# Optimization experiments

Measured on AMD Instinct MI355X. Metric: run time of the kernel, lower is better.

## Reference

```python
import jax, jax.numpy as jnp
import numpy as np

N, E, D_IN, D_OUT, K = 50000, 800000, 128, 128, 3

def setup_inputs() -> dict:
    key = jax.random.key(0)
    k1, k2, k3, k4, k5 = jax.random.split(key, 5)
    feat = jax.random.normal(k1, (N, D_IN), dtype=jnp.float32)
    src = jax.random.randint(k2, (E,), 0, N)
    dst = jax.random.randint(k3, (E,), 0, N)
    theta = 0.1 * jax.random.normal(k4, (K + 1,), dtype=jnp.float32)
    # xavier-uniform-like linear weight [out, in]
    lim = float(np.sqrt(6.0 / (D_IN + D_OUT)))
    W = jax.random.uniform(k5, (D_OUT, D_IN), minval=-lim, maxval=lim, dtype=jnp.float32)
    return {"feat": feat, "src": src, "dst": dst, "theta": theta, "W": W}

def reference(feat, src, dst, theta, W):
    n = feat.shape[0]
    # in-degree per destination node, clamped to >= 1
    deg = jax.ops.segment_sum(jnp.ones_like(dst, dtype=feat.dtype), dst, num_segments=n)
    d_invsqrt = jnp.maximum(deg, 1.0) ** -0.5  # [N]
    d_invsqrt = d_invsqrt[:, None]

    def L_prime(x):
        # -D^{-1/2} A D^{-1/2} x  (A aggregates src -> dst)
        msg = (x * d_invsqrt)[src]                      # [E, D]
        agg = jax.ops.segment_sum(msg, dst, num_segments=n)
        return -agg * d_invsqrt

    k = theta.shape[0] - 1
    h = theta[0] * feat
    T_km2 = feat
    T_km1 = L_prime(feat)
    if k >= 1:
        h = h + theta[1] * (T_km1 + 1.0) * 0.5
    for order in range(2, k + 1):
        T_k = 2.0 * L_prime(T_km1) - T_km2
        h = h + theta[order] * (T_k + 1.0) * 0.5
        T_km2, T_km1 = T_km1, T_k

    out = h @ W.T  # linear, no bias
    return jax.nn.leaky_relu(out, negative_slope=0.01)
```

## Files before the change

### kernel.cpp

```cpp
#include <hip/hip_runtime.h>

#define NN 50000
#define EE 800000
#define D 128

static inline size_t align_up(size_t x, size_t a) { return (x + a - 1) & ~(a - 1); }

__device__ __forceinline__ unsigned pack_bf16(float a, float b) {
    unsigned ua = __float_as_uint(a), ub = __float_as_uint(b);
    unsigned ra = (ua + 0x7fffu + ((ua >> 16) & 1u)) >> 16;
    unsigned rb = (ub + 0x7fffu + ((ub >> 16) & 1u)) & 0xffff0000u;
    return ra | rb;
}
__device__ __forceinline__ float bf_lo(unsigned u) { return __uint_as_float(u << 16); }
__device__ __forceinline__ float bf_hi(unsigned u) { return __uint_as_float(u & 0xffff0000u); }

__global__ void deg_kernel(const int* __restrict__ dst, int* __restrict__ deg, int E) {
    int e = blockIdx.x * blockDim.x + threadIdx.x;
    if (e < E) atomicAdd(&deg[dst[e]], 1);
}

__global__ void dinv_kernel(const int* __restrict__ deg, float* __restrict__ dinv, int n) {
    int i = blockIdx.x * blockDim.x + threadIdx.x;
    if (i < n) {
        float d = (float)deg[i];
        dinv[i] = rsqrtf(d > 1.0f ? d : 1.0f);
    }
}

__global__ void scale_kernel(const float* __restrict__ feat, const float* __restrict__ dinv,
                             unsigned* __restrict__ featb, int n) {
    int idx = blockIdx.x * blockDim.x + threadIdx.x;
    if (idx >= n * 64) return;
    int i = idx >> 6;
    float di = dinv[i];
    float2 f = ((const float2*)feat)[idx];
    featb[idx] = pack_bf16(f.x * di, f.y * di);
}

__global__ void scan_blk_kernel(const int* __restrict__ deg, int* __restrict__ bscan,
                                int* __restrict__ btot, int n) {
    __shared__ int ws4[4];
    int tid = threadIdx.x, b = blockIdx.x;
    int i = b * 256 + tid;
    int v = (i < n) ? deg[i] : 0;
    int lane = tid & 63, w = tid >> 6;
    int sc = v;
    #pragma unroll
    for (int off = 1; off < 64; off <<= 1) {
        int t = __shfl_up(sc, off);
        if (lane >= off) sc += t;
    }
    if (lane == 63) ws4[w] = sc;
    __syncthreads();
    int woff = 0;
    #pragma unroll
    for (int k = 0; k < 4; ++k)
        if (k < w) woff += ws4[k];
    int inc = sc + woff;
    bscan[b * 256 + tid] = inc;
    if (tid == 255) btot[b] = inc;
}

__global__ void scan_top_kernel(int* __restrict__ btot, int nb) {
    __shared__ int ws4[4];
    int tid = threadIdx.x;
    int v = (tid < nb) ? btot[tid] : 0;
    int lane = tid & 63, w = tid >> 6;
    int sc = v;
    #pragma unroll
    for (int off = 1; off < 64; off <<= 1) {
        int t = __shfl_up(sc, off);
        if (lane >= off) sc += t;
    }
    if (lane == 63) ws4[w] = sc;
    __syncthreads();
    int woff = 0;
    #pragma unroll
    for (int k = 0; k < 4; ++k)
        if (k < w) woff += ws4[k];
    if (tid < nb) btot[tid] = sc + woff - v;
}

__global__ void scan_fix_kernel(const int* __restrict__ bscan, const int* __restrict__ btot,
                                const int* __restrict__ deg, int* __restrict__ rowptr,
                                int* __restrict__ cursor, int n) {
    int i = blockIdx.x * blockDim.x + threadIdx.x;
    if (i >= n) return;
    int inc = bscan[i] + btot[i >> 8];
    rowptr[i + 1] = inc;
    cursor[i] = inc - deg[i];
    if (i == 0) rowptr[0] = 0;
}

__global__ void scatter_kernel(const int* __restrict__ src, const int* __restrict__ dst,
                               int* __restrict__ cursor, int* __restrict__ csr_src, int E) {
    int e = blockIdx.x * blockDim.x + threadIdx.x;
    if (e < E) {
        int p = atomicAdd(&cursor[dst[e]], 1);
        csr_src[p] = src[e];
    }
}

template <int MODE>
__global__ __launch_bounds__(256) void agg_kernel(
    const int* __restrict__ rowptr, const int* __restrict__ csr_src,
    const float* __restrict__ dinv, const unsigned* __restrict__ Xb,
    const float* __restrict__ feat, const float* __restrict__ T1f,
    const float* __restrict__ T2f, const float* __restrict__ theta,
    float* __restrict__ outf, unsigned* __restrict__ outb, int n) {
    int wid = (blockIdx.x * blockDim.x + threadIdx.x) >> 6;
    int lane = threadIdx.x & 63;
    if (wid >= n) return;
    int half = lane >> 5;
    int hl = lane & 31;
    int beg = rowptr[wid];
    int end = rowptr[wid + 1];
    const uint2* X2 = (const uint2*)Xb;
    float a0 = 0.f, a1 = 0.f, a2 = 0.f, a3 = 0.f;
    for (int e0 = beg; e0 < end; e0 += 64) {
        int s = (e0 + lane < end) ? csr_src[e0 + lane] : 0;
        int cnt = min(64, end - e0);
        int j = 0;
        for (; j + 8 <= cnt; j += 8) {
            int s0 = __shfl(s, j + 0 + half);
            int s1 = __shfl(s, j + 2 + half);
            int s2 = __shfl(s, j + 4 + half);
            int s3 = __shfl(s, j + 6 + half);
            uint2 u0 = X2[(size_t)s0 * 32 + hl];
            uint2 u1 = X2[(size_t)s1 * 32 + hl];
            uint2 u2 = X2[(size_t)s2 * 32 + hl];
            uint2 u3 = X2[(size_t)s3 * 32 + hl];
            a0 += bf_lo(u0.x); a1 += bf_hi(u0.x); a2 += bf_lo(u0.y); a3 += bf_hi(u0.y);
            a0 += bf_lo(u1.x); a1 += bf_hi(u1.x); a2 += bf_lo(u1.y); a3 += bf_hi(u1.y);
            a0 += bf_lo(u2.x); a1 += bf_hi(u2.x); a2 += bf_lo(u2.y); a3 += bf_hi(u2.y);
            a0 += bf_lo(u3.x); a1 += bf_hi(u3.x); a2 += bf_lo(u3.y); a3 += bf_hi(u3.y);
        }
        for (; j + 2 <= cnt; j += 2) {
            int sj = __shfl(s, j + half);
            uint2 u = X2[(size_t)sj * 32 + hl];
            a0 += bf_lo(u.x); a1 += bf_hi(u.x); a2 += bf_lo(u.y); a3 += bf_hi(u.y);
        }
        if (j < cnt) {
            int sj = __shfl(s, j);
            if (half == 0) {
                uint2 u = X2[(size_t)sj * 32 + hl];
                a0 += bf_lo(u.x); a1 += bf_hi(u.x); a2 += bf_lo(u.y); a3 += bf_hi(u.y);
            }
        }
    }
    a0 += __shfl_xor(a0, 32);
    a1 += __shfl_xor(a1, 32);
    a2 += __shfl_xor(a2, 32);
    a3 += __shfl_xor(a3, 32);

    float di = dinv[wid];
    size_t row4 = (size_t)wid * 32 + hl;
    float r0, r1, r2, r3;
    if (MODE == 1) {
        r0 = -di * a0; r1 = -di * a1; r2 = -di * a2; r3 = -di * a3;
    } else if (MODE == 2) {
        float4 f = ((const float4*)feat)[row4];
        r0 = -2.f * di * a0 - f.x;
        r1 = -2.f * di * a1 - f.y;
        r2 = -2.f * di * a2 - f.z;
        r3 = -2.f * di * a3 - f.w;
    } else {
        float4 f = ((const float4*)feat)[row4];
        float4 t1 = ((const float4*)T1f)[row4];
        float4 t2 = ((const float4*)T2f)[row4];
        float th0 = theta[0], th1 = theta[1], th2 = theta[2], th3 = theta[3];
        float c = 0.5f * (th1 + th2 + th3);
        float t30 = -2.f * di * a0 - t1.x;
        float t31 = -2.f * di * a1 - t1.y;
        float t32 = -2.f * di * a2 - t1.z;
        float t33 = -2.f * di * a3 - t1.w;
        r0 = th0 * f.x + 0.5f * (th1 * t1.x + th2 * t2.x + th3 * t30) + c;
        r1 = th0 * f.y + 0.5f * (th1 * t1.y + th2 * t2.y + th3 * t31) + c;
        r2 = th0 * f.z + 0.5f * (th1 * t1.z + th2 * t2.z + th3 * t32) + c;
        r3 = th0 * f.w + 0.5f * (th1 * t1.w + th2 * t2.w + th3 * t33) + c;
    }
    if (half == 0) {
        ((float4*)outf)[row4] = make_float4(r0, r1, r2, r3);
    } else if (MODE != 3) {
        uint2 p;
        p.x = pack_bf16(r0 * di, r1 * di);
        p.y = pack_bf16(r2 * di, r3 * di);
        ((uint2*)outb)[row4] = p;
    }
}

#define BK 32
#define TS 68
__global__ __launch_bounds__(256) void gemm_kernel(const float* __restrict__ h,
                                                   const float* __restrict__ W,
                                                   float* __restrict__ out, int n) {
    __shared__ float hs[BK * TS];
    __shared__ float ws[BK * TS];
    int tid = threadIdx.x;
    int tile = blockIdx.x >> 1;
    int o0 = (blockIdx.x & 1) * 64;
    int node0 = tile * 64;
    int tx = tid & 15, ty = tid >> 4;

    float acc[4][4] = {};

    for (int k0 = 0; k0 < D; k0 += BK) {
        __syncthreads();
        #pragma unroll
        for (int p = 0; p < 2; ++p) {
            int idx = p * 256 + tid;
            int r = idx >> 3, c4 = idx & 7;
            int nn = node0 + r;
            float4 v = make_float4(0.f, 0.f, 0.f, 0.f);
            if (nn < n) v = ((const float4*)(h + (size_t)nn * D + k0))[c4];
            hs[(c4 * 4 + 0) * TS + r] = v.x;
            hs[(c4 * 4 + 1) * TS + r] = v.y;
            hs[(c4 * 4 + 2) * TS + r] = v.z;
            hs[(c4 * 4 + 3) * TS + r] = v.w;
            float4 wv = ((const float4*)(W + (size_t)(o0 + r) * D + k0))[c4];
            ws[(c4 * 4 + 0) * TS + r] = wv.x;
            ws[(c4 * 4 + 1) * TS + r] = wv.y;
            ws[(c4 * 4 + 2) * TS + r] = wv.z;
            ws[(c4 * 4 + 3) * TS + r] = wv.w;
        }
        __syncthreads();
        #pragma unroll
        for (int kk = 0; kk < BK; ++kk) {
            float4 hv = *(const float4*)&hs[kk * TS + 4 * ty];
            float4 wv = *(const float4*)&ws[kk * TS + 4 * tx];
            float hvv[4] = {hv.x, hv.y, hv.z, hv.w};
            float wvv[4] = {wv.x, wv.y, wv.z, wv.w};
            #pragma unroll
            for (int k = 0; k < 4; ++k)
                #pragma unroll
                for (int kk2 = 0; kk2 < 4; ++kk2)
                    acc[k][kk2] = fmaf(hvv[k], wvv[kk2], acc[k][kk2]);
        }
    }

    #pragma unroll
    for (int k = 0; k < 4; ++k) {
        int nn = node0 + 4 * ty + k;
        if (nn < n) {
            float4 r4;
            r4.x = acc[k][0] > 0.f ? acc[k][0] : 0.01f * acc[k][0];
            r4.y = acc[k][1] > 0.f ? acc[k][1] : 0.01f * acc[k][1];
            r4.z = acc[k][2] > 0.f ? acc[k][2] : 0.01f * acc[k][2];
            r4.w = acc[k][3] > 0.f ? acc[k][3] : 0.01f * acc[k][3];
            ((float4*)(out + (size_t)nn * D + o0))[tx] = r4;
        }
    }
}

extern "C" void kernel_launch(void* const* d_in, const int* in_sizes, int n_in,
                              void* d_out, int out_size, void* d_ws, size_t ws_size,
                              hipStream_t stream) {
    const float* feat = (const float*)d_in[0];
    const int* src = (const int*)d_in[1];
    const int* dst = (const int*)d_in[2];
    const float* theta = (const float*)d_in[3];
    const float* W = (const float*)d_in[4];
    float* out = (float*)d_out;

    const int n = NN;
    const int E = EE;
    const int nb = (n + 255) / 256;

    char* w = (char*)d_ws;
    size_t off = 0;
    int* deg = (int*)(w + off); off = align_up(off + (size_t)n * 4, 512);
    float* dinv = (float*)(w + off); off = align_up(off + (size_t)n * 4, 512);
    int* rowptr = (int*)(w + off); off = align_up(off + (size_t)(n + 1) * 4, 512);
    int* cursor = (int*)(w + off); off = align_up(off + (size_t)n * 4, 512);
    int* bscan = (int*)(w + off); off = align_up(off + (size_t)(nb * 256) * 4, 512);
    int* btot = (int*)(w + off); off = align_up(off + (size_t)256 * 4, 512);
    int* csr_src = (int*)(w + off); off = align_up(off + (size_t)E * 4, 512);
    unsigned* featb = (unsigned*)(w + off); off = align_up(off + (size_t)n * 64 * 4, 512);
    float* T1f = (float*)(w + off); off = align_up(off + (size_t)n * D * 4, 512);
    unsigned* T1b = (unsigned*)(w + off); off = align_up(off + (size_t)n * 64 * 4, 512);
    float* T2f = (float*)(w + off); off = align_up(off + (size_t)n * D * 4, 512);
    unsigned* T2b = (unsigned*)(w + off); off = align_up(off + (size_t)n * 64 * 4, 512);
    (void)ws_size;

    hipMemsetAsync(deg, 0, (size_t)n * 4, stream);

    deg_kernel<<<(E + 255) / 256, 256, 0, stream>>>(dst, deg, E);
    dinv_kernel<<<(n + 255) / 256, 256, 0, stream>>>(deg, dinv, n);
    scale_kernel<<<(n * 64 + 255) / 256, 256, 0, stream>>>(feat, dinv, featb, n);
    scan_blk_kernel<<<nb, 256, 0, stream>>>(deg, bscan, btot, n);
    scan_top_kernel<<<1, 256, 0, stream>>>(btot, nb);
    scan_fix_kernel<<<(n + 255) / 256, 256, 0, stream>>>(bscan, btot, deg, rowptr, cursor, n);
    scatter_kernel<<<(E + 255) / 256, 256, 0, stream>>>(src, dst, cursor, csr_src, E);

    int agg_grid = (n + 3) / 4;
    agg_kernel<1><<<agg_grid, 256, 0, stream>>>(rowptr, csr_src, dinv, featb, feat, T1f, T2f, theta, T1f, T1b, n);
    agg_kernel<2><<<agg_grid, 256, 0, stream>>>(rowptr, csr_src, dinv, T1b, feat, T1f, T2f, theta, T2f, T2b, n);
    agg_kernel<3><<<agg_grid, 256, 0, stream>>>(rowptr, csr_src, dinv, T2b, feat, T1f, T2f, theta, T1f, (unsigned*)0, n);

    int gemm_grid = ((n + 63) / 64) * 2;
    gemm_kernel<<<gemm_grid, 256, 0, stream>>>(T1f, W, out, n);
}
```

Baseline: 250.6 us.

## Partition degree and scatter atomics by destination range per XCD

Rewrites the degree-count and CSR scatter kernels so each block handles only destinations in one of eight node ranges, chosen by blockIdx modulo 8. The aim is to keep atomic updates to a given slice of the counter array on one die/L2, avoiding cross-die atomic contention. In exchange every edge index is read eight times, and the partition size is hardcoded to the node count.

```diff
diff --git a/kernel.cpp b/kernel.cpp
--- a/kernel.cpp
+++ b/kernel.cpp
@@ -3,6 +3,7 @@
 #define NN 50000
 #define EE 800000
 #define D 128
+#define PARTSZ 6250
 
 static inline size_t align_up(size_t x, size_t a) { return (x + a - 1) & ~(a - 1); }
 
@@ -15,9 +16,19 @@
 __device__ __forceinline__ float bf_lo(unsigned u) { return __uint_as_float(u << 16); }
 __device__ __forceinline__ float bf_hi(unsigned u) { return __uint_as_float(u & 0xffff0000u); }
 
-__global__ void deg_kernel(const int* __restrict__ dst, int* __restrict__ deg, int E) {
-    int e = blockIdx.x * blockDim.x + threadIdx.x;
-    if (e < E) atomicAdd(&deg[dst[e]], 1);
+__global__ __launch_bounds__(256) void deg_kernel(const int* __restrict__ dst,
+                                                  int* __restrict__ deg, int E) {
+    int part = blockIdx.x & 7;
+    int nch = gridDim.x >> 3;
+    int chunk = blockIdx.x >> 3;
+    int per = (E + nch - 1) / nch;
+    int beg = chunk * per;
+    int end = min(E, beg + per);
+    int plo = part * PARTSZ, phi = plo + PARTSZ;
+    for (int e = beg + threadIdx.x; e < end; e += 256) {
+        int d = dst[e];
+        if (d >= plo && d < phi) atomicAdd(&deg[d], 1);
+    }
 }
 
 __global__ void dinv_kernel(const int* __restrict__ deg, float* __restrict__ dinv, int n) {
@@ -93,12 +104,24 @@
     if (i == 0) rowptr[0] = 0;
 }
 
-__global__ void scatter_kernel(const int* __restrict__ src, const int* __restrict__ dst,
-                               int* __restrict__ cursor, int* __restrict__ csr_src, int E) {
-    int e = blockIdx.x * blockDim.x + threadIdx.x;
-    if (e < E) {
-        int p = atomicAdd(&cursor[dst[e]], 1);
-        csr_src[p] = src[e];
+__global__ __launch_bounds__(256) void scatter_kernel(const int* __restrict__ src,
+                                                      const int* __restrict__ dst,
+                                                      int* __restrict__ cursor,
+                                                      int* __restrict__ csr_src, int E) {
+    int part = blockIdx.x & 7;
+    int nch = gridDim.x >> 3;
+    int chunk = blockIdx.x >> 3;
+    int per = (E + nch - 1) / nch;
+    int beg = chunk * per;
+    int end = min(E, beg + per);
+    int plo = part * PARTSZ, phi = plo + PARTSZ;
+    for (int e = beg + threadIdx.x; e < end; e += 256) {
+        int d = dst[e];
+        int s = src[e];
+        if (d >= plo && d < phi) {
+            int p = atomicAdd(&cursor[d], 1);
+            csr_src[p] = s;
+        }
     }
 }
 
@@ -285,13 +308,13 @@
 
     hipMemsetAsync(deg, 0, (size_t)n * 4, stream);
 
-    deg_kernel<<<(E + 255) / 256, 256, 0, stream>>>(dst, deg, E);
+    deg_kernel<<<2048, 256, 0, stream>>>(dst, deg, E);
     dinv_kernel<<<(n + 255) / 256, 256, 0, stream>>>(deg, dinv, n);
     scale_kernel<<<(n * 64 + 255) / 256, 256, 0, stream>>>(feat, dinv, featb, n);
     scan_blk_kernel<<<nb, 256, 0, stream>>>(deg, bscan, btot, n);
     scan_top_kernel<<<1, 256, 0, stream>>>(btot, nb);
     scan_fix_kernel<<<(n + 255) / 256, 256, 0, stream>>>(bscan, btot, deg, rowptr, cursor, n);
-    scatter_kernel<<<(E + 255) / 256, 256, 0, stream>>>(src, dst, cursor, csr_src, E);
+    scatter_kernel<<<2048, 256, 0, stream>>>(src, dst, cursor, csr_src, E);
 
     int agg_grid = (n + 3) / 4;
     agg_kernel<1><<<agg_grid, 256, 0, stream>>>(rowptr, csr_src, dinv, featb, feat, T1f, T2f, theta, T1f, T1b, n);
```

Result: faster. 238.5 us (-4.8%).
